# Performance work log

Hardware: AMD Instinct MI355X
Metric: run time of the kernel (lower is better)

## Reference

```python
import jax, jax.numpy as jnp
import numpy as np

N_NODES = 50000
N_EDGES = 800000
N_FEAT = 128
NHID = 64
B = 512          # num graphs
K = 30           # sort-pool k
N_CLASSES = 10


def _sage(x, src, dst, Wl, bl, Wr, n):
    # PyG SAGEConv: out = lin_l(mean_{j in N(i)} x_j) + lin_r(x_i)
    deg = jax.ops.segment_sum(jnp.ones(src.shape[0], x.dtype), dst, num_segments=n)
    agg = jax.ops.segment_sum(x[src], dst, num_segments=n)
    agg = agg / jnp.maximum(deg, 1.0)[:, None]
    return agg @ Wl + bl + x @ Wr


def _sort_pool(x, batch, num_graphs, k):
    # sort nodes within each graph descending by last feature channel, keep top-k (zero pad)
    n, f = x.shape
    order = jnp.lexsort((-x[:, -1], batch))  # primary: batch asc, secondary: last-feat desc
    xs = x[order]
    bs = batch[order]
    counts = jax.ops.segment_sum(jnp.ones(n, jnp.int32), batch, num_segments=num_graphs)
    starts = jnp.concatenate([jnp.zeros(1, jnp.int32), jnp.cumsum(counts)[:-1]])
    rank = jnp.arange(n, dtype=jnp.int32) - starts[bs]
    valid = rank < k
    gidx = jnp.where(valid, bs, num_graphs)  # out-of-bounds -> dropped by scatter
    ridx = jnp.where(valid, rank, 0)
    out = jnp.zeros((num_graphs, k, f), x.dtype).at[gidx, ridx].set(xs)
    return out  # [B, k, f]


def setup_inputs() -> dict:
    key = jax.random.key(0)
    ks = jax.random.split(key, 16)
    d = {}
    d["x"] = jax.random.normal(ks[0], (N_NODES, N_FEAT), dtype=jnp.float32)
    d["edge_index"] = jax.random.randint(ks[1], (2, N_EDGES), 0, N_NODES, dtype=jnp.int64)
    d["batch"] = jnp.sort(jax.random.randint(ks[2], (N_NODES,), 0, B, dtype=jnp.int64))

    def lin(k, fan_in, shape):
        s = 1.0 / np.sqrt(fan_in)
        return jax.random.uniform(k, shape, jnp.float32, -s, s)

    d["W1l"] = lin(ks[3], N_FEAT, (N_FEAT, NHID)); d["b1"] = lin(ks[4], N_FEAT, (NHID,))
    d["W1r"] = lin(ks[5], N_FEAT, (N_FEAT, NHID))
    d["W2l"] = lin(ks[6], NHID, (NHID, NHID)); d["b2"] = lin(ks[7], NHID, (NHID,))
    d["W2r"] = lin(ks[8], NHID, (NHID, NHID))
    d["W3l"] = lin(ks[9], NHID, (NHID, NHID)); d["b3"] = lin(ks[10], NHID, (NHID,))
    d["W3r"] = lin(ks[11], NHID, (NHID, NHID))
    d["convw"] = lin(ks[12], NHID * 5, (32, NHID, 5))  # OIH
    d["convb"] = lin(ks[13], NHID * 5, (32,))
    d["lin1w"] = lin(ks[14], 32 * 26, (32 * 26, NHID)); d["lin1b"] = lin(ks[14], 32 * 26, (NHID,))
    d["lin2w"] = lin(ks[15], NHID, (NHID, N_CLASSES)); d["lin2b"] = lin(ks[15], NHID, (N_CLASSES,))
    return d


def reference(x, edge_index, batch, W1l, b1, W1r, W2l, b2, W2r, W3l, b3, W3r,
              convw, convb, lin1w, lin1b, lin2w, lin2b):
    src, dst = edge_index[0], edge_index[1]
    h = jax.nn.relu(_sage(x, src, dst, W1l, b1, W1r, N_NODES))
    h = jax.nn.relu(_sage(h, src, dst, W2l, b2, W2r, N_NODES))
    h = jax.nn.relu(_sage(h, src, dst, W3l, b3, W3r, N_NODES))
    p = _sort_pool(h, batch, B, K)            # [B, K, NHID]
    p = jnp.transpose(p, (0, 2, 1))           # [B, NHID, K]
    c = jax.lax.conv_general_dilated(p, convw, (1,), 'VALID',
                                     dimension_numbers=('NCH', 'OIH', 'NCH'))
    c = jax.nn.relu(c + convb[None, :, None])  # [B, 32, 26]
    f = c.reshape(B, -1)
    f = jax.nn.relu(f @ lin1w + lin1b)
    logits = f @ lin2w + lin2b
    return jax.nn.log_softmax(logits, axis=-1)
```

## Files before the change

kernel.cpp:

```cpp
#include <hip/hip_runtime.h>
#include <hip/hip_bf16.h>
#include <math.h>

#define NND 50000
#define NE 800000
#define NF 128
#define NH 64
#define NB 512
#define KP 30
#define NCLS 10
#define NBKT 49
#define NTILE 196
#define NG1 782
#define NSET 208

typedef __hip_bfloat16 bf16;
typedef unsigned long long u64;
typedef unsigned short ushort_t;
typedef __attribute__((ext_vector_type(8))) short bf16x8;
typedef __attribute__((ext_vector_type(4))) float f32x4;

__device__ __forceinline__ float ldF(const void* p, size_t i, int isbf){
    return isbf ? __bfloat162float(((const bf16*)p)[i]) : ((const float*)p)[i];
}

__device__ __forceinline__ ushort_t f2bf(float v){
    unsigned u = __float_as_uint(v);
    unsigned r = u + 0x7FFFu + ((u >> 16) & 1u);
    return (ushort_t)(r >> 16);
}

__device__ __forceinline__ int floatsAreBf16(const unsigned* __restrict__ xw, int tid){
    unsigned w = xw[tid & 63];
    int ex = (int)((w >> 7) & 0xFF);
    u64 m = __ballot(ex >= 100 && ex <= 140);
    return __popcll(m) >= 32;
}
__device__ __forceinline__ int intsAreI64(const int* __restrict__ ew, int tid){
    u64 m = __ballot(ew[2*(tid & 63) + 1] == 0);
    return __popcll(m) >= 48;
}

__device__ __forceinline__ int edgeSrc(const int* ei, int e, int i64){
    return i64 ? ei[2*e] : ei[e];
}
__device__ __forceinline__ int edgeDst(const int* ei, int e, int i64){
    return i64 ? ei[2*NE + 2*e] : ei[NE + e];
}

__global__ __launch_bounds__(256) void k1_kernel(
    const unsigned* __restrict__ xw, const int* __restrict__ ei,
    const int* __restrict__ batch, int* __restrict__ starts,
    const void* W1l, const void* W1r, const void* b1,
    const void* W2l, const void* W2r, const void* b2,
    const void* W3l, const void* W3r, const void* b3,
    const void* convw, const void* convb,
    const void* l1w, const void* l1b, const void* l2w, const void* l2b,
    ushort_t* __restrict__ wB1, ushort_t* __restrict__ wB2, ushort_t* __restrict__ wB3,
    float* __restrict__ b1f, float* __restrict__ b2f, float* __restrict__ b3f,
    float* __restrict__ wT, float* __restrict__ cbf,
    float* __restrict__ l1wf, float* __restrict__ l1bf,
    float* __restrict__ l2wf, float* __restrict__ l2bf,
    int* __restrict__ bcnt, int* __restrict__ dctr,
    int* __restrict__ bbase, int* __restrict__ bcur, int* __restrict__ offs)
{
    int tid = threadIdx.x;
    if (blockIdx.x < NTILE){
        __shared__ int lh[NBKT];
        __shared__ int sc[NBKT];
        __shared__ int lastFlag;
        int i64 = intsAreI64(ei, tid);
        if (tid < NBKT) lh[tid] = 0;
        __syncthreads();
        int t0 = blockIdx.x*4096;
        #pragma unroll 4
        for (int k = 0; k < 16; ++k){
            int e = t0 + k*256 + tid;
            if (e < NE) atomicAdd(&lh[edgeDst(ei,e,i64) >> 10], 1);
        }
        __syncthreads();
        if (tid < NBKT && lh[tid]) atomicAdd(&bcnt[tid], lh[tid]);
        __syncthreads();
        if (tid == 0){
            __threadfence();
            int old = atomicAdd(dctr, 1);
            lastFlag = (old == NTILE-1) ? 1 : 0;
        }
        __syncthreads();
        if (lastFlag){
            if (tid < NBKT) sc[tid] = atomicAdd(&bcnt[tid], 0);
            __syncthreads();
            if (tid == 0){
                int acc = 0;
                for (int b = 0; b < NBKT; ++b){
                    bbase[b] = acc; bcur[b] = acc; acc += sc[b];
                }
                bbase[NBKT] = acc;
                offs[NND] = NE;
            }
        }
    } else {
        int wbf = floatsAreBf16(xw, tid);
        int i64 = intsAreI64(ei, tid);
        int i = (blockIdx.x - NTILE)*256 + tid;
        if (i < NND){
            int b  = i64 ? batch[2*i] : batch[i];
            int pb = (i == 0) ? -1 : (i64 ? batch[2*(i-1)] : batch[i-1]);
            for (int g = pb+1; g <= b; ++g) starts[g] = i;
            if (i == NND-1) for (int g = b+1; g <= NB; ++g) starts[g] = NND;
        }
        {
            int j = i & 7, lane = (i >> 3) & 63, t = (i >> 9) & 7, c = i >> 12;
            int k = c*32 + (lane >> 4)*8 + j;
            int n = t*16 + (lane & 15);
            if (i < 16384){
                float v = (n < 64) ? ldF(W1l, (size_t)k*NH + n, wbf)
                                   : ldF(W1r, (size_t)k*NH + (n-64), wbf);
                wB1[i] = f2bf(v);
            }
            if (i < 8192){
                float v2 = (n < 64) ? ldF(W2l, (size_t)k*NH + n, wbf)
                                    : ldF(W2r, (size_t)k*NH + (n-64), wbf);
                float v3 = (n < 64) ? ldF(W3l, (size_t)k*NH + n, wbf)
                                    : ldF(W3r, (size_t)k*NH + (n-64), wbf);
                wB2[i] = f2bf(v2);
                wB3[i] = f2bf(v3);
            }
        }
        if (i < 64){
            b1f[i] = ldF(b1, i, wbf);
            b2f[i] = ldF(b2, i, wbf);
            b3f[i] = ldF(b3, i, wbf);
            l1bf[i] = ldF(l1b, i, wbf);
        }
        if (i < 10240){
            int o = i / 320, rem = i - o*320, ch = rem/5, h = rem - ch*5;
            wT[ch*160 + h*32 + o] = ldF(convw, i, wbf);
        }
        if (i < 53248) l1wf[i] = ldF(l1w, i, wbf);
        if (i < 640)   l2wf[i] = ldF(l2w, i, wbf);
        if (i < 32)    cbf[i]  = ldF(convb, i, wbf);
        if (i < 10)    l2bf[i] = ldF(l2b, i, wbf);
    }
}

__global__ __launch_bounds__(256) void k2_kernel(
    const void* __restrict__ x, const int* __restrict__ ei,
    const ushort_t* __restrict__ wB1, const float* __restrict__ b1f,
    ushort_t* __restrict__ ybf, float* __restrict__ z,
    int* __restrict__ bcur, int2* __restrict__ bedges)
{
    int tid = threadIdx.x;
    if (blockIdx.x < NG1){
        constexpr int K = NF, KC = K/32, RS = K + 8;
        __shared__ ushort_t hA[64*RS];
        int isbf = floatsAreBf16((const unsigned*)x, tid);
        int base = blockIdx.x * 64;
        for (int i = tid; i < 64*K; i += 256){
            int r = i / K, c = i - r*K;
            int node = base + r;
            float v = (node < NND) ? ldF(x, (size_t)node*K + c, isbf) : 0.f;
            hA[r*RS + c] = f2bf(v);
        }
        __syncthreads();
        int lane = tid & 63, w = tid >> 6;
        int n16 = lane & 15, quad = lane >> 4;
        f32x4 acc[8];
        #pragma unroll
        for (int t = 0; t < 8; ++t) acc[t] = (f32x4){0.f,0.f,0.f,0.f};
        const bf16x8* bp = (const bf16x8*)wB1;
        #pragma unroll
        for (int c = 0; c < KC; ++c){
            bf16x8 a = *(const bf16x8*)&hA[(w*16 + n16)*RS + c*32 + quad*8];
            #pragma unroll
            for (int t = 0; t < 8; ++t){
                bf16x8 b = bp[(c*8 + t)*64 + lane];
                acc[t] = __builtin_amdgcn_mfma_f32_16x16x32_bf16(a, b, acc[t], 0, 0, 0);
            }
        }
        #pragma unroll
        for (int t = 0; t < 8; ++t){
            int f = (t & 3)*16 + n16;
            float bv = (t >= 4) ? b1f[f] : 0.f;
            #pragma unroll
            for (int r = 0; r < 4; ++r){
                int node = base + w*16 + quad*4 + r;
                if (node < NND){
                    if (t < 4) ybf[(size_t)node*NH + f] = f2bf(acc[t][r]);
                    else       z[(size_t)node*NH + f] = acc[t][r] + bv;
                }
            }
        }
    } else {
        __shared__ int lh[NBKT];
        __shared__ int lcur[NBKT];
        int i64 = intsAreI64(ei, tid);
        if (tid < NBKT) lh[tid] = 0;
        __syncthreads();
        int t0 = (blockIdx.x - NG1)*4096;
        int myd[16], mys[16];
        int cnt = 0;
        #pragma unroll 4
        for (int k = 0; k < 16; ++k){
            int e = t0 + k*256 + tid;
            if (e < NE){
                int d = edgeDst(ei,e,i64), s_ = edgeSrc(ei,e,i64);
                myd[cnt] = d; mys[cnt] = s_; ++cnt;
                atomicAdd(&lh[d >> 10], 1);
            }
        }
        __syncthreads();
        if (tid < NBKT) lcur[tid] = lh[tid] ? atomicAdd(&bcur[tid], lh[tid]) : 0;
        __syncthreads();
        for (int k = 0; k < cnt; ++k){
            int b = myd[k] >> 10;
            int p = atomicAdd(&lcur[b], 1);
            bedges[p] = make_int2(mys[k], myd[k]);
        }
    }
}

__global__ __launch_bounds__(1024) void csr_finalize(const int2* __restrict__ bedges,
                                                     const int* __restrict__ bbase,
                                                     int* __restrict__ offs,
                                                     int* __restrict__ csr){
    __shared__ int hist[1024];
    int b = blockIdx.x;
    int tid = threadIdx.x;
    int dst0 = b << 10;
    int nd = NND - dst0; if (nd > 1024) nd = 1024;
    int e0 = bbase[b], e1 = bbase[b+1];
    hist[tid] = 0;
    __syncthreads();
    for (int e = e0 + tid; e < e1; e += 1024)
        atomicAdd(&hist[bedges[e].y - dst0], 1);
    __syncthreads();
    int own = hist[tid];
    for (int st = 1; st < 1024; st <<= 1){
        int v = (tid >= st) ? hist[tid-st] : 0;
        __syncthreads();
        hist[tid] += v;
        __syncthreads();
    }
    int excl = hist[tid] - own;
    if (tid < nd) offs[dst0 + tid] = e0 + excl;
    __syncthreads();
    hist[tid] = excl;
    __syncthreads();
    for (int e = e0 + tid; e < e1; e += 1024){
        int2 ed = bedges[e];
        int p = atomicAdd(&hist[ed.y - dst0], 1);
        csr[e0 + p] = ed.x;
    }
}

__device__ __forceinline__ void addbf8(uint4 u, float* a){
    a[0] += __uint_as_float(u.x << 16);
    a[1] += __uint_as_float(u.x & 0xFFFF0000u);
    a[2] += __uint_as_float(u.y << 16);
    a[3] += __uint_as_float(u.y & 0xFFFF0000u);
    a[4] += __uint_as_float(u.z << 16);
    a[5] += __uint_as_float(u.z & 0xFFFF0000u);
    a[6] += __uint_as_float(u.w << 16);
    a[7] += __uint_as_float(u.w & 0xFFFF0000u);
}

__global__ __launch_bounds__(256) void gather_mfma(
    const ushort_t* __restrict__ yb, const int* __restrict__ offs,
    const int* __restrict__ csr, const float* __restrict__ z,
    const ushort_t* __restrict__ wB, const float* __restrict__ bfp,
    ushort_t* __restrict__ ybf_out, float* __restrict__ z_out,
    ushort_t* __restrict__ ykey_out)
{
    constexpr int K = NH;
    constexpr int KC = K/32;
    constexpr int RS = K + 8;
    __shared__ ushort_t hA[64*RS];
    int tid = threadIdx.x;
    int base = blockIdx.x * 64;

    {
        int nl = tid >> 2, q = tid & 3;
        int node = base + nl;
        float acc[16];
        #pragma unroll
        for (int i = 0; i < 16; ++i) acc[i] = 0.f;
        ushort_t row[16];
        if (node < NND){
            int o0 = offs[node], o1 = offs[node+1];
            int e = o0;
            for (; e + 3 < o1; e += 4){
                int s0 = csr[e], s1 = csr[e+1], s2 = csr[e+2], s3 = csr[e+3];
                const uint4* p0 = (const uint4*)&yb[(size_t)s0*NH + q*16];
                const uint4* p1 = (const uint4*)&yb[(size_t)s1*NH + q*16];
                const uint4* p2 = (const uint4*)&yb[(size_t)s2*NH + q*16];
                const uint4* p3 = (const uint4*)&yb[(size_t)s3*NH + q*16];
                uint4 a0 = p0[0], a1 = p0[1], b0 = p1[0], b1 = p1[1];
                uint4 c0 = p2[0], c1 = p2[1], d0 = p3[0], d1 = p3[1];
                addbf8(a0, acc); addbf8(a1, acc+8);
                addbf8(b0, acc); addbf8(b1, acc+8);
                addbf8(c0, acc); addbf8(c1, acc+8);
                addbf8(d0, acc); addbf8(d1, acc+8);
            }
            for (; e < o1; ++e){
                const uint4* p0 = (const uint4*)&yb[(size_t)csr[e]*NH + q*16];
                uint4 a0 = p0[0], a1 = p0[1];
                addbf8(a0, acc); addbf8(a1, acc+8);
            }
            float dd = (float)(o1 - o0); dd = dd > 1.f ? dd : 1.f;
            float inv = 1.f / dd;
            const float4* zp = (const float4*)&z[(size_t)node*NH + q*16];
            #pragma unroll
            for (int i4 = 0; i4 < 4; ++i4){
                float4 zz = zp[i4];
                float v0 = acc[i4*4+0]*inv + zz.x;
                float v1 = acc[i4*4+1]*inv + zz.y;
                float v2 = acc[i4*4+2]*inv + zz.z;
                float v3 = acc[i4*4+3]*inv + zz.w;
                row[i4*4+0] = f2bf(v0 > 0.f ? v0 : 0.f);
                row[i4*4+1] = f2bf(v1 > 0.f ? v1 : 0.f);
                row[i4*4+2] = f2bf(v2 > 0.f ? v2 : 0.f);
                row[i4*4+3] = f2bf(v3 > 0.f ? v3 : 0.f);
            }
        } else {
            #pragma unroll
            for (int i = 0; i < 16; ++i) row[i] = 0;
        }
        unsigned pk[8];
        #pragma unroll
        for (int i = 0; i < 8; ++i)
            pk[i] = (unsigned)row[2*i] | ((unsigned)row[2*i+1] << 16);
        *(uint4*)&hA[nl*RS + q*16]     = make_uint4(pk[0],pk[1],pk[2],pk[3]);
        *(uint4*)&hA[nl*RS + q*16 + 8] = make_uint4(pk[4],pk[5],pk[6],pk[7]);
    }
    __syncthreads();

    int lane = tid & 63, w = tid >> 6;
    int n16 = lane & 15, quad = lane >> 4;
    f32x4 acc[8];
    #pragma unroll
    for (int t = 0; t < 8; ++t) acc[t] = (f32x4){0.f,0.f,0.f,0.f};
    const bf16x8* bp = (const bf16x8*)wB;
    #pragma unroll
    for (int c = 0; c < KC; ++c){
        bf16x8 a = *(const bf16x8*)&hA[(w*16 + n16)*RS + c*32 + quad*8];
        #pragma unroll
        for (int t = 0; t < 8; ++t){
            bf16x8 b = bp[(c*8 + t)*64 + lane];
            acc[t] = __builtin_amdgcn_mfma_f32_16x16x32_bf16(a, b, acc[t], 0, 0, 0);
        }
    }
    #pragma unroll
    for (int t = 0; t < 8; ++t){
        int f = (t & 3)*16 + n16;
        float bv = (t >= 4) ? bfp[f] : 0.f;
        #pragma unroll
        for (int r = 0; r < 4; ++r){
            int node = base + w*16 + quad*4 + r;
            if (node < NND){
                if (t < 4){
                    ushort_t yv = f2bf(acc[t][r]);
                    ybf_out[(size_t)node*NH + f] = yv;
                    if (ykey_out != nullptr && t == 3 && n16 == 15)
                        ykey_out[node] = yv;
                } else {
                    z_out[(size_t)node*NH + f] = acc[t][r] + bv;
                }
            }
        }
    }
}

__device__ __forceinline__ void acc4(uint2 u, float& a0, float& a1, float& a2, float& a3){
    a0 += __uint_as_float(u.x << 16);
    a1 += __uint_as_float(u.x & 0xFFFF0000u);
    a2 += __uint_as_float(u.y << 16);
    a3 += __uint_as_float(u.y & 0xFFFF0000u);
}

__global__ __launch_bounds__(256) void head4_kernel(
    const ushort_t* __restrict__ yb, const ushort_t* __restrict__ ykey,
    const int* __restrict__ offs, const int* __restrict__ csr,
    const float* __restrict__ z, const int* __restrict__ starts,
    const float* __restrict__ wT, const float* __restrict__ cbf,
    const float* __restrict__ l1wf, const float* __restrict__ l1bf,
    const float* __restrict__ l2wf, const float* __restrict__ l2bf,
    float* __restrict__ outp)
{
    __shared__ u64  keys[256];
    __shared__ int  sel[KP];
    __shared__ float pT[64*32];
    __shared__ float part[8*832];
    __shared__ float cbuf[832];
    __shared__ float fbuf[NH];
    __shared__ float logitsS[NCLS];
    int g = blockIdx.x, tid = threadIdx.x;
    int s = starts[g], e = starts[g+1];
    int cnt = e - s; if (cnt > 256) cnt = 256; if (cnt < 0) cnt = 0;

    u64 key = 0xFFFFFFFFFFFFFFFFull;
    if (tid < cnt){
        int node = s + tid;
        int o0 = offs[node], o1 = offs[node+1];
        float a = 0.f;
        int ee = o0;
        for (; ee + 3 < o1; ee += 4){
            float v0 = __uint_as_float((unsigned)ykey[csr[ee+0]] << 16);
            float v1 = __uint_as_float((unsigned)ykey[csr[ee+1]] << 16);
            float v2 = __uint_as_float((unsigned)ykey[csr[ee+2]] << 16);
            float v3 = __uint_as_float((unsigned)ykey[csr[ee+3]] << 16);
            a += v0; a += v1; a += v2; a += v3;
        }
        for (; ee < o1; ++ee)
            a += __uint_as_float((unsigned)ykey[csr[ee]] << 16);
        float dd = (float)(o1 - o0); dd = dd > 1.f ? dd : 1.f;
        float inv = 1.f / dd;
        float v = a*inv + z[(size_t)node*NH + 63];
        v = v > 0.f ? v : 0.f;
        unsigned u = __float_as_uint(v);
        unsigned m = (u & 0x80000000u) ? ~u : (u | 0x80000000u);
        unsigned d = ~m;
        key = ((u64)d << 32) | (unsigned)tid;
    }
    keys[tid] = key;
    __syncthreads();
    for (int k = 2; k <= 256; k <<= 1){
        for (int j = k >> 1; j > 0; j >>= 1){
            int partner = tid ^ j;
            u64 a = keys[tid], b = keys[partner];
            bool up = ((tid & k) == 0);
            bool amin = a < b;
            u64 keep;
            if (partner > tid) keep = (up == amin) ? a : b;
            else               keep = (up == amin) ? b : a;
            __syncthreads();
            keys[tid] = keep;
            __syncthreads();
        }
    }
    if (tid < KP){
        u64 kk = keys[tid];
        sel[tid] = ((unsigned)(kk >> 32) == 0xFFFFFFFFu) ? -1 : (int)(kk & 0xFFFFFFFFu);
    }
    if (tid < 64){ pT[tid*32 + 30] = 0.f; pT[tid*32 + 31] = 0.f; }
    __syncthreads();

    #pragma unroll
    for (int r0 = 0; r0 < 32; r0 += 16){
        int r = r0 + (tid >> 4);
        int q = tid & 15;
        if (r < KP){
            float4 v = make_float4(0.f,0.f,0.f,0.f);
            int li = sel[r];
            if (li >= 0){
                int node = s + li;
                int o0 = offs[node], o1 = offs[node+1];
                float a0=0.f, a1=0.f, a2=0.f, a3=0.f;
                int ee = o0;
                for (; ee + 3 < o1; ee += 4){
                    int s0 = csr[ee], s1 = csr[ee+1], s2 = csr[ee+2], s3 = csr[ee+3];
                    uint2 u0 = *(const uint2*)&yb[(size_t)s0*NH + q*4];
                    uint2 u1 = *(const uint2*)&yb[(size_t)s1*NH + q*4];
                    uint2 u2 = *(const uint2*)&yb[(size_t)s2*NH + q*4];
                    uint2 u3 = *(const uint2*)&yb[(size_t)s3*NH + q*4];
                    acc4(u0, a0,a1,a2,a3); acc4(u1, a0,a1,a2,a3);
                    acc4(u2, a0,a1,a2,a3); acc4(u3, a0,a1,a2,a3);
                }
                for (; ee < o1; ++ee){
                    uint2 u = *(const uint2*)&yb[(size_t)csr[ee]*NH + q*4];
                    acc4(u, a0,a1,a2,a3);
                }
                float dd = (float)(o1 - o0); dd = dd > 1.f ? dd : 1.f;
                float inv = 1.f / dd;
                float4 zz = *(const float4*)&z[(size_t)node*NH + q*4];
                v.x = a0*inv + zz.x; v.y = a1*inv + zz.y;
                v.z = a2*inv + zz.z; v.w = a3*inv + zz.w;
                v.x = v.x > 0.f ? v.x : 0.f;  v.y = v.y > 0.f ? v.y : 0.f;
                v.z = v.z > 0.f ? v.z : 0.f;  v.w = v.w > 0.f ? v.w : 0.f;
            }
            pT[(q*4+0)*32 + r] = v.x;
            pT[(q*4+1)*32 + r] = v.y;
            pT[(q*4+2)*32 + r] = v.z;
            pT[(q*4+3)*32 + r] = v.w;
        }
    }
    __syncthreads();

    int o = tid & 31, chg = tid >> 5;
    float acc[26];
    #pragma unroll
    for (int t = 0; t < 26; ++t) acc[t] = 0.f;
    for (int c8 = 0; c8 < 8; ++c8){
        int ch = chg*8 + c8;
        const float4* prow = (const float4*)&pT[ch*32];
        float p[32];
        #pragma unroll
        for (int q = 0; q < 8; ++q){
            float4 v = prow[q];
            p[4*q]=v.x; p[4*q+1]=v.y; p[4*q+2]=v.z; p[4*q+3]=v.w;
        }
        const float* wrow = &wT[ch*160 + o];
        #pragma unroll
        for (int h = 0; h < 5; ++h){
            float wv = wrow[h*32];
            #pragma unroll
            for (int t = 0; t < 26; ++t) acc[t] += p[t+h]*wv;
        }
    }
    #pragma unroll
    for (int t = 0; t < 26; ++t) part[chg*832 + o*26 + t] = acc[t];
    __syncthreads();

    for (int i = tid; i < 832; i += 256){
        int oo = i / 26;
        float a = cbf[oo];
        #pragma unroll
        for (int cg = 0; cg < 8; ++cg) a += part[cg*832 + i];
        cbuf[i] = a > 0.f ? a : 0.f;
    }
    __syncthreads();

    {
        int p = tid >> 6, j = tid & 63;
        float a = 0.f;
        int m0 = p*208;
        #pragma unroll 4
        for (int m = m0; m < m0 + 208; ++m)
            a += cbuf[m] * l1wf[(size_t)m*NH + j];
        part[p*NH + j] = a;
    }
    __syncthreads();
    if (tid < NH){
        float v = part[tid] + part[NH+tid] + part[2*NH+tid] + part[3*NH+tid] + l1bf[tid];
        fbuf[tid] = v > 0.f ? v : 0.f;
    }
    __syncthreads();
    if (tid < NCLS){
        float a = l2bf[tid];
        #pragma unroll
        for (int j = 0; j < NH; ++j) a += fbuf[j] * l2wf[j*NCLS + tid];
        logitsS[tid] = a;
    }
    __syncthreads();
    if (tid == 0){
        float m = logitsS[0];
        for (int c = 1; c < NCLS; ++c) m = fmaxf(m, logitsS[c]);
        float ssum = 0.f;
        for (int c = 0; c < NCLS; ++c) ssum += expf(logitsS[c]-m);
        float lse = m + logf(ssum);
        for (int c = 0; c < NCLS; ++c)
            outp[(size_t)g*NCLS + c] = logitsS[c] - lse;
    }
}

extern "C" void kernel_launch(void* const* d_in, const int* in_sizes, int n_in,
                              void* d_out, int out_size, void* d_ws, size_t ws_size,
                              hipStream_t stream) {
    const void* x    = d_in[0];
    const int*  ei   = (const int*)d_in[1];
    const int*  batch= (const int*)d_in[2];
    const void *W1l=d_in[3], *b1=d_in[4],  *W1r=d_in[5];
    const void *W2l=d_in[6], *b2=d_in[7],  *W2r=d_in[8];
    const void *W3l=d_in[9], *b3=d_in[10], *W3r=d_in[11];
    const void *convw=d_in[12], *convb=d_in[13];
    const void *l1w=d_in[14], *l1b=d_in[15];
    const void *l2w=d_in[16], *l2b=d_in[17];
    float* out = (float*)d_out;

    float* wsf = (float*)d_ws;
    ushort_t* yA = (ushort_t*)wsf;
    float* zA  = wsf + (size_t)NND*NH/2;
    ushort_t* yB = (ushort_t*)(zA + (size_t)NND*NH);
    float* zB  = (float*)(yB + (size_t)NND*NH);
    int2* bedges = (int2*)(zB + (size_t)NND*NH);
    ushort_t* wB1 = (ushort_t*)(bedges + NE);
    ushort_t* wB2 = wB1 + 16384;
    ushort_t* wB3 = wB2 + 8192;
    ushort_t* ykey = wB3 + 8192;
    float* b1f  = (float*)(ykey + NND + 8);
    float* b2f  = b1f + 64;
    float* b3f  = b2f + 64;
    float* wT   = b3f + 64;
    float* cbf  = wT + 10240;
    float* l1wf = cbf + 32;
    float* l1bf = l1wf + 53248;
    float* l2wf = l1bf + 64;
    float* l2bf = l2wf + 640;
    int* starts = (int*)(l2bf + 16);
    int* bcnt   = starts + 520;
    int* dctr   = bcnt + NBKT;
    int* bbase  = bcnt + 64;
    int* bcur   = bbase + 64;
    int* offs   = bcur + 64;
    int* csr    = offs + NND + 3;

    (void)hipMemsetAsync(bcnt, 0, 50*sizeof(int), stream);

    k1_kernel<<<NTILE + NSET, 256, 0, stream>>>(
        (const unsigned*)x, ei, batch, starts,
        W1l, W1r, b1, W2l, W2r, b2, W3l, W3r, b3,
        convw, convb, l1w, l1b, l2w, l2b,
        wB1, wB2, wB3, b1f, b2f, b3f,
        wT, cbf, l1wf, l1bf, l2wf, l2bf,
        bcnt, dctr, bbase, bcur, offs);

    k2_kernel<<<NG1 + NTILE, 256, 0, stream>>>(
        x, ei, wB1, b1f, yA, zA, bcur, bedges);

    csr_finalize<<<NBKT, 1024, 0, stream>>>(bedges, bbase, offs, csr);

    gather_mfma<<<NG1, 256, 0, stream>>>(yA, offs, csr, zA, wB2, b2f, yB, zB, nullptr);
    gather_mfma<<<NG1, 256, 0, stream>>>(yB, offs, csr, zB, wB3, b3f, yA, zA, ykey);

    head4_kernel<<<NB, 256, 0, stream>>>(yA, ykey, offs, csr, zA, starts,
                                         wT, cbf, l1wf, l1bf, l2wf, l2bf, out);
}
```

Before: 261.4 us.

## Widen head kernel to 512 threads and use wave shuffles in bitonic sort

The per-graph head kernel now launches 512 threads. The bitonic sort keeps each key in a register and exchanges partners with 64-lane shuffles when the stride is under 64, so it needs LDS and barriers only for the larger strides. The top-k gather now fits in a single pass, the conv1d and lin1 stages are split over twice as many threads, and the transposed pool buffer uses a padded stride of 33 to reduce LDS bank conflicts. The trade-off is higher register and occupancy pressure from the larger block, and a larger share of the sort runs on threads whose keys are only padding.

```diff
diff --git a/kernel.cpp b/kernel.cpp
--- a/kernel.cpp
+++ b/kernel.cpp
@@ -378,7 +378,14 @@
     a3 += __uint_as_float(u.y & 0xFFFF0000u);
 }
 
-__global__ __launch_bounds__(256) void head4_kernel(
+__device__ __forceinline__ u64 shflx64(u64 v, int m){
+    int lo = __shfl_xor((int)(unsigned)v, m, 64);
+    int hi = __shfl_xor((int)(unsigned)(v >> 32), m, 64);
+    return ((u64)(unsigned)hi << 32) | (unsigned)lo;
+}
+
+#define PSTR 33
+__global__ __launch_bounds__(512, 4) void head4_kernel(
     const ushort_t* __restrict__ yb, const ushort_t* __restrict__ ykey,
     const int* __restrict__ offs, const int* __restrict__ csr,
     const float* __restrict__ z, const int* __restrict__ starts,
@@ -387,9 +394,9 @@
     const float* __restrict__ l2wf, const float* __restrict__ l2bf,
     float* __restrict__ outp)
 {
-    __shared__ u64  keys[256];
-    __shared__ int  sel[KP];
-    __shared__ float pT[64*32];
+    __shared__ u64  keysL[512];
+    __shared__ int  sel[32];
+    __shared__ float pT[64*PSTR];
     __shared__ float part[8*832];
     __shared__ float cbuf[832];
     __shared__ float fbuf[NH];
@@ -422,32 +429,29 @@
         unsigned d = ~m;
         key = ((u64)d << 32) | (unsigned)tid;
     }
-    keys[tid] = key;
-    __syncthreads();
+
     for (int k = 2; k <= 256; k <<= 1){
         for (int j = k >> 1; j > 0; j >>= 1){
-            int partner = tid ^ j;
-            u64 a = keys[tid], b = keys[partner];
-            bool up = ((tid & k) == 0);
-            bool amin = a < b;
-            u64 keep;
-            if (partner > tid) keep = (up == amin) ? a : b;
-            else               keep = (up == amin) ? b : a;
-            __syncthreads();
-            keys[tid] = keep;
-            __syncthreads();
-        }
-    }
-    if (tid < KP){
-        u64 kk = keys[tid];
-        sel[tid] = ((unsigned)(kk >> 32) == 0xFFFFFFFFu) ? -1 : (int)(kk & 0xFFFFFFFFu);
-    }
-    if (tid < 64){ pT[tid*32 + 30] = 0.f; pT[tid*32 + 31] = 0.f; }
-    __syncthreads();
-
-    #pragma unroll
-    for (int r0 = 0; r0 < 32; r0 += 16){
-        int r = r0 + (tid >> 4);
+            u64 other;
+            if (j >= 64){
+                keysL[tid] = key;
+                __syncthreads();
+                other = keysL[tid ^ j];
+            } else {
+                other = shflx64(key, j);
+            }
+            bool keepMin = (((tid & j) == 0) == ((tid & k) == 0));
+            bool less = key < other;
+            key = (keepMin == less) ? key : other;
+            if (j >= 64) __syncthreads();
+        }
+    }
+    if (tid < KP)
+        sel[tid] = (((unsigned)(key >> 32)) == 0xFFFFFFFFu) ? -1 : (int)(key & 0xFFFFFFFFu);
+    __syncthreads();
+
+    {
+        int r = tid >> 4;
         int q = tid & 15;
         if (r < KP){
             float4 v = make_float4(0.f,0.f,0.f,0.f);
@@ -478,40 +482,39 @@
                 v.x = v.x > 0.f ? v.x : 0.f;  v.y = v.y > 0.f ? v.y : 0.f;
                 v.z = v.z > 0.f ? v.z : 0.f;  v.w = v.w > 0.f ? v.w : 0.f;
             }
-            pT[(q*4+0)*32 + r] = v.x;
-            pT[(q*4+1)*32 + r] = v.y;
-            pT[(q*4+2)*32 + r] = v.z;
-            pT[(q*4+3)*32 + r] = v.w;
-        }
-    }
-    __syncthreads();
-
-    int o = tid & 31, chg = tid >> 5;
-    float acc[26];
-    #pragma unroll
-    for (int t = 0; t < 26; ++t) acc[t] = 0.f;
-    for (int c8 = 0; c8 < 8; ++c8){
-        int ch = chg*8 + c8;
-        const float4* prow = (const float4*)&pT[ch*32];
-        float p[32];
-        #pragma unroll
-        for (int q = 0; q < 8; ++q){
-            float4 v = prow[q];
-            p[4*q]=v.x; p[4*q+1]=v.y; p[4*q+2]=v.z; p[4*q+3]=v.w;
-        }
-        const float* wrow = &wT[ch*160 + o];
-        #pragma unroll
-        for (int h = 0; h < 5; ++h){
-            float wv = wrow[h*32];
+            pT[(q*4+0)*PSTR + r] = v.x;
+            pT[(q*4+1)*PSTR + r] = v.y;
+            pT[(q*4+2)*PSTR + r] = v.z;
+            pT[(q*4+3)*PSTR + r] = v.w;
+        }
+    }
+    __syncthreads();
+
+    {
+        int o = tid & 31, th = (tid >> 5) & 1, chg = tid >> 6;
+        int tbase = th*13;
+        float acc[13];
+        #pragma unroll
+        for (int t = 0; t < 13; ++t) acc[t] = 0.f;
+        for (int c8 = 0; c8 < 8; ++c8){
+            int ch = chg*8 + c8;
+            float p[17];
             #pragma unroll
-            for (int t = 0; t < 26; ++t) acc[t] += p[t+h]*wv;
-        }
-    }
-    #pragma unroll
-    for (int t = 0; t < 26; ++t) part[chg*832 + o*26 + t] = acc[t];
-    __syncthreads();
-
-    for (int i = tid; i < 832; i += 256){
+            for (int i = 0; i < 17; ++i) p[i] = pT[ch*PSTR + tbase + i];
+            const float* wrow = &wT[ch*160 + o];
+            #pragma unroll
+            for (int h = 0; h < 5; ++h){
+                float wv = wrow[h*32];
+                #pragma unroll
+                for (int t = 0; t < 13; ++t) acc[t] += p[t+h]*wv;
+            }
+        }
+        #pragma unroll
+        for (int t = 0; t < 13; ++t) part[chg*832 + o*26 + tbase + t] = acc[t];
+    }
+    __syncthreads();
+
+    for (int i = tid; i < 832; i += 512){
         int oo = i / 26;
         float a = cbf[oo];
         #pragma unroll
@@ -521,17 +524,20 @@
     __syncthreads();
 
     {
-        int p = tid >> 6, j = tid & 63;
+        int p8 = tid >> 6, j = tid & 63;
         float a = 0.f;
-        int m0 = p*208;
+        int m0 = p8*104;
         #pragma unroll 4
-        for (int m = m0; m < m0 + 208; ++m)
+        for (int m = m0; m < m0 + 104; ++m)
             a += cbuf[m] * l1wf[(size_t)m*NH + j];
-        part[p*NH + j] = a;
+        part[p8*NH + j] = a;
     }
     __syncthreads();
     if (tid < NH){
-        float v = part[tid] + part[NH+tid] + part[2*NH+tid] + part[3*NH+tid] + l1bf[tid];
+        float v = part[tid];
+        #pragma unroll
+        for (int p8 = 1; p8 < 8; ++p8) v += part[p8*NH + tid];
+        v += l1bf[tid];
         fbuf[tid] = v > 0.f ? v : 0.f;
     }
     __syncthreads();
@@ -612,6 +618,6 @@
     gather_mfma<<<NG1, 256, 0, stream>>>(yA, offs, csr, zA, wB2, b2f, yB, zB, nullptr);
     gather_mfma<<<NG1, 256, 0, stream>>>(yB, offs, csr, zB, wB3, b3f, yA, zA, ykey);
 
-    head4_kernel<<<NB, 256, 0, stream>>>(yA, ykey, offs, csr, zA, starts,
+    head4_kernel<<<NB, 512, 0, stream>>>(yA, ykey, offs, csr, zA, starts,
                                          wT, cbf, l1wf, l1bf, l2wf, l2bf, out);
 }
```

Measured after the change: 247.7 us. 5.2% less time.
